# Performance work log

Hardware: AMD Instinct MI355X
Metric: run time of the kernel (lower is better)

## Reference

```python
import jax, jax.numpy as jnp
import numpy as np

B, N, E, H = 32, 256, 768, 12
D = E // H
SCALING = D ** -0.5


def setup_inputs() -> dict:
    key = jax.random.key(0)
    ks = jax.random.split(key, 10)
    inp = {
        "query": jax.random.normal(ks[0], (B, N, E), dtype=jnp.float32),
        "attn_bias": jax.random.normal(ks[1], (B * H, N, N), dtype=jnp.float32),
        "delta_pos": jax.random.normal(ks[2], (B, N, N, 3), dtype=jnp.float32),
        # Linear params stored as (in, out) so y = x @ W + b (equivalent to torch Linear).
        "Wq": jax.random.normal(ks[3], (E, E), dtype=jnp.float32) * 0.02,
        "bq": jnp.zeros((E,), dtype=jnp.float32),
        "Wk": jax.random.normal(ks[4], (E, E), dtype=jnp.float32) * 0.02,
        "bk": jnp.zeros((E,), dtype=jnp.float32),
        "Wv": jax.random.normal(ks[5], (E, E), dtype=jnp.float32) * 0.02,
        "bv": jnp.zeros((E,), dtype=jnp.float32),
        # force_proj: Linear(E, 1, bias=False) -> weight vector (E,)
        "wf": jax.random.normal(ks[6], (E,), dtype=jnp.float32) * 0.02,
    }
    return inp


def reference(query, attn_bias, delta_pos, Wq, bq, Wk, bk, Wv, bv, wf):
    b, n, e = query.shape
    h, d = H, D
    # QKV projections -> (b, n, h, d)
    q = (query @ Wq + bq).reshape(b, n, h, d) * SCALING
    k = (query @ Wk + bk).reshape(b, n, h, d)
    v = (query @ Wv + bv).reshape(b, n, h, d)
    # attention scores (b, h, n, n)
    attn = jnp.einsum("bnhd,bmhd->bhnm", q, k)
    # add bias on flattened (b*h, n, n), softmax over last dim (dropout=0.1 disabled: eval mode)
    probs = jax.nn.softmax(attn.reshape(b * h, n, n) + attn_bias, axis=-1)
    probs = probs.reshape(b, h, n, n)
    # equivariant weighted sum: x[b,n,c,h,d] = sum_m probs[b,h,n,m] * delta_pos[b,n,m,c] * v[b,m,h,d]
    x = jnp.einsum("bhnm,bnmc,bmhd->bnchd", probs, delta_pos, v)
    x = x.reshape(b, n, 3, e)
    # force projection (shared Linear(E,1,bias=False) applied per spatial component)
    force = jnp.einsum("bnce,e->bnc", x, wf).astype(jnp.float32)
    return force
```

## Files before the change

### kernel.cpp

```cpp
#include <hip/hip_runtime.h>
#include <hip/hip_bf16.h>

#define Bc 32
#define Nc 256
#define Ec 768
#define Hc 12
#define Dc 64

typedef __attribute__((ext_vector_type(8))) __bf16 bf16x8;
typedef __attribute__((ext_vector_type(8))) unsigned short u16x8;
typedef __attribute__((ext_vector_type(4))) float f32x4;

__device__ __forceinline__ unsigned short f2bf(float x) {
  union { float f; unsigned u; } v; v.f = x;
  unsigned r = v.u + 0x7fff + ((v.u >> 16) & 1);
  return (unsigned short)(r >> 16);
}

#define GL2LDS(gp, lp) __builtin_amdgcn_global_load_lds( \
    (__attribute__((address_space(1))) void*)(gp),        \
    (__attribute__((address_space(3))) void*)(lp), 16, 0, 0)

__global__ __launch_bounds__(256) void k_trans(const float* __restrict__ Wq,
                                               const float* __restrict__ Wk,
                                               unsigned short* __restrict__ WT) {
  __shared__ float tile[32][33];
  const float* W = blockIdx.z ? Wk : Wq;
  float scale = blockIdx.z ? 1.0f : 0.125f;
  int rowoff = blockIdx.z ? Ec : 0;
  int k0 = blockIdx.x * 32, n0 = blockIdx.y * 32;
  int r = threadIdx.x >> 5, c = threadIdx.x & 31;
  #pragma unroll
  for (int it = 0; it < 4; ++it)
    tile[r + 8 * it][c] = W[(k0 + r + 8 * it) * Ec + n0 + c];
  __syncthreads();
  #pragma unroll
  for (int it = 0; it < 4; ++it)
    WT[(rowoff + n0 + r + 8 * it) * Ec + k0 + c] = f2bf(scale * tile[c][r + 8 * it]);
}

__global__ void k_build_wvf(const float* __restrict__ Wv, const float* __restrict__ bv,
                            const float* __restrict__ wf,
                            const float* __restrict__ bq, const float* __restrict__ bk,
                            float* __restrict__ Wvf, float* __restrict__ bvf,
                            float* __restrict__ bb) {
  int idx = blockIdx.x * 256 + threadIdx.x;
  if (idx < Ec * Hc) {
    int e = idx / Hc, h = idx % Hc;
    float s = 0.f;
    for (int d = 0; d < Dc; ++d) s += Wv[e * Ec + h * Dc + d] * wf[h * Dc + d];
    Wvf[idx] = s;
  }
  if (idx < Hc) {
    float s = 0.f;
    for (int d = 0; d < Dc; ++d) s += bv[idx * Dc + d] * wf[idx * Dc + d];
    bvf[idx] = s;
  }
  if (idx < 2 * Ec)
    bb[idx] = (idx < Ec) ? 0.125f * bq[idx] : bk[idx - Ec];
}

__global__ __launch_bounds__(256) void k_vf(const float* __restrict__ query,
                                            const float* __restrict__ Wvf,
                                            const float* __restrict__ bvf,
                                            float* __restrict__ vfT,
                                            unsigned short* __restrict__ Xb) {
  __shared__ float wl[Ec * 13];
  __shared__ float bl[Hc];
  for (int i = threadIdx.x; i < Ec * Hc; i += 256) {
    int e = i / Hc, h = i % Hc;
    wl[e * 13 + h] = Wvf[i];
  }
  if (threadIdx.x < Hc) bl[threadIdx.x] = bvf[threadIdx.x];
  __syncthreads();
  int warp = threadIdx.x >> 6, lane = threadIdx.x & 63;
  int r = blockIdx.x * 4 + warp;
  float q[12];
  #pragma unroll
  for (int i = 0; i < 12; ++i) q[i] = query[r * Ec + lane + 64 * i];
  #pragma unroll
  for (int i = 0; i < 12; ++i) Xb[r * Ec + lane + 64 * i] = f2bf(q[i]);
  int b = r >> 8, m = r & 255;
  for (int h = 0; h < Hc; ++h) {
    float s = 0.f;
    #pragma unroll
    for (int i = 0; i < 12; ++i) s += q[i] * wl[(lane + 64 * i) * 13 + h];
    #pragma unroll
    for (int off = 32; off; off >>= 1) s += __shfl_xor(s, off);
    if (lane == 0) vfT[(b * Hc + h) * Nc + m] = s + bl[h];
  }
}

__global__ __launch_bounds__(256) void k_gemm_qk(const unsigned short* __restrict__ Xb,
                                                 const unsigned short* __restrict__ WT,
                                                 const float* __restrict__ bb,
                                                 unsigned short* __restrict__ QK) {
  __shared__ unsigned short As[128 * 64];
  __shared__ unsigned short Bs[128 * 64];
  int wgid = (blockIdx.x & 7) * 96 + (blockIdx.x >> 3);
  int bm = wgid & 63, bn = wgid >> 6;
  int t = threadIdx.x;
  int wave = t >> 6, lane = t & 63;
  int wr = wave >> 1, wc = wave & 1;
  int lrow = lane & 15, lq = lane >> 4;
  const int row0 = bm * 128, col0 = bn * 128;

  int srow = wave * 8 + (lane >> 3);
  int soct = (lane & 7);

  f32x4 acc[4][4];
  #pragma unroll
  for (int m = 0; m < 4; ++m)
    #pragma unroll
    for (int n = 0; n < 4; ++n) acc[m][n] = f32x4{0.f, 0.f, 0.f, 0.f};

  for (int ks = 0; ks < Ec; ks += 64) {
    #pragma unroll
    for (int i = 0; i < 4; ++i) {
      int r = i * 32 + srow;
      int go = soct ^ (r & 7);
      GL2LDS(Xb + (row0 + r) * Ec + ks + go * 8, As + i * 2048 + wave * 512);
      GL2LDS(WT + (col0 + r) * Ec + ks + go * 8, Bs + i * 2048 + wave * 512);
    }
    __syncthreads();
    bf16x8 af[4][2], bfg[4][2];
    #pragma unroll
    for (int m = 0; m < 4; ++m) {
      int ra = wr * 64 + m * 16 + lrow;
      #pragma unroll
      for (int kk = 0; kk < 2; ++kk) {
        int o = kk * 4 + lq;
        af[m][kk] = *(const bf16x8*)(As + ra * 64 + ((o ^ (ra & 7)) << 3));
      }
    }
    #pragma unroll
    for (int n = 0; n < 4; ++n) {
      int rb = wc * 64 + n * 16 + lrow;
      #pragma unroll
      for (int kk = 0; kk < 2; ++kk) {
        int o = kk * 4 + lq;
        bfg[n][kk] = *(const bf16x8*)(Bs + rb * 64 + ((o ^ (rb & 7)) << 3));
      }
    }
    #pragma unroll
    for (int kk = 0; kk < 2; ++kk)
      #pragma unroll
      for (int m = 0; m < 4; ++m)
        #pragma unroll
        for (int n = 0; n < 4; ++n)
          acc[m][n] = __builtin_amdgcn_mfma_f32_16x16x32_bf16(af[m][kk], bfg[n][kk], acc[m][n], 0, 0, 0);
    __syncthreads();
  }
  int crow = lq * 4, ccol = lane & 15;
  #pragma unroll
  for (int m = 0; m < 4; ++m)
    #pragma unroll
    for (int n = 0; n < 4; ++n) {
      int col = col0 + wc * 64 + n * 16 + ccol;
      float bias = bb[col];
      #pragma unroll
      for (int j = 0; j < 4; ++j) {
        int row = row0 + wr * 64 + m * 16 + crow + j;
        QK[row * 1536 + col] = f2bf(acc[m][n][j] + bias);
      }
    }
}

__global__ __launch_bounds__(256) void k_attn(const unsigned short* __restrict__ QK,
                                              const float* __restrict__ bias,
                                              const float* __restrict__ vfT,
                                              const float* __restrict__ delta,
                                              float* __restrict__ fpart) {
  __shared__ float S[16 * 256];

  int bi = blockIdx.x;
  int xcd = bi & 7, slot = bi >> 3;
  int b = xcd * 4 + (slot >> 6);
  int rem = slot & 63;
  int nt = rem >> 2, hg = rem & 3;
  int n0 = nt * 16;
  int h0 = hg * 3;

  int t = threadIdx.x, w = t >> 6, l = t & 63;
  int lq = l >> 4, lr = l & 15;

  float w_reg[4][4];
  #pragma unroll
  for (int p = 0; p < 4; ++p)
    #pragma unroll
    for (int i = 0; i < 4; ++i) w_reg[p][i] = 0.f;

  const unsigned short* Qbase = QK + (size_t)b * Nc * 1536;
  const unsigned short* Kbase = Qbase + 768;

  float4 bias4[4], vf4;
  {
    const float* bp = bias + (size_t)(b * Hc + h0) * Nc * Nc;
    #pragma unroll
    for (int p = 0; p < 4; ++p)
      bias4[p] = *(const float4*)(bp + (n0 + w * 4 + p) * Nc + l * 4);
    vf4 = *(const float4*)(vfT + (size_t)(b * Hc + h0) * Nc + l * 4);
  }

  #pragma unroll 1
  for (int hh = 0; hh < 3; ++hh) {
    int h = h0 + hh;
    bf16x8 qf[2];
    #pragma unroll
    for (int kk = 0; kk < 2; ++kk)
      qf[kk] = *(const bf16x8*)(Qbase + (n0 + lr) * 1536 + h * 64 + kk * 32 + lq * 8);
    f32x4 acc[4];
    #pragma unroll
    for (int mf = 0; mf < 4; ++mf) acc[mf] = f32x4{0.f, 0.f, 0.f, 0.f};
    #pragma unroll
    for (int mf = 0; mf < 4; ++mf)
      #pragma unroll
      for (int kk = 0; kk < 2; ++kk) {
        bf16x8 af = *(const bf16x8*)(Kbase + (w * 64 + mf * 16 + lr) * 1536 + h * 64 + kk * 32 + lq * 8);
        acc[mf] = __builtin_amdgcn_mfma_f32_16x16x32_bf16(af, qf[kk], acc[mf], 0, 0, 0);
      }
    float4 bias_nx[4], vf_nx;
    if (hh < 2) {
      const float* bpn = bias + (size_t)(b * Hc + h + 1) * Nc * Nc;
      #pragma unroll
      for (int p = 0; p < 4; ++p)
        bias_nx[p] = *(const float4*)(bpn + (n0 + w * 4 + p) * Nc + l * 4);
      vf_nx = *(const float4*)(vfT + (size_t)(b * Hc + h + 1) * Nc + l * 4);
    }
    #pragma unroll
    for (int mf = 0; mf < 4; ++mf) {
      int m0 = w * 64 + mf * 16 + lq * 4;
      *(f32x4*)&S[lr * 256 + (m0 ^ ((lr & 7) << 2))] = acc[mf];
    }
    __syncthreads();
    #pragma unroll
    for (int p = 0; p < 4; ++p) {
      int r = w * 4 + p;
      float4 sv = *(const float4*)&S[r * 256 + ((l * 4) ^ ((r & 7) << 2))];
      float p0 = __expf(sv.x + bias4[p].x);
      float p1 = __expf(sv.y + bias4[p].y);
      float p2 = __expf(sv.z + bias4[p].z);
      float p3 = __expf(sv.w + bias4[p].w);
      float ssum = (p0 + p1) + (p2 + p3);
      #pragma unroll
      for (int off = 1; off < 64; off <<= 1) ssum += __shfl_xor(ssum, off);
      float inv = 1.f / ssum;
      w_reg[p][0] += p0 * inv * vf4.x;
      w_reg[p][1] += p1 * inv * vf4.y;
      w_reg[p][2] += p2 * inv * vf4.z;
      w_reg[p][3] += p3 * inv * vf4.w;
    }
    __syncthreads();
    if (hh < 2) {
      #pragma unroll
      for (int p = 0; p < 4; ++p) bias4[p] = bias_nx[p];
      vf4 = vf_nx;
    }
  }
  #pragma unroll
  for (int p = 0; p < 4; ++p) {
    int r = w * 4 + p, n = n0 + r;
    const float* dp = delta + ((size_t)(b * Nc + n) * Nc + l * 4) * 3;
    float4 d0 = *(const float4*)(dp);
    float4 d1 = *(const float4*)(dp + 4);
    float4 d2 = *(const float4*)(dp + 8);
    float w0 = w_reg[p][0], w1 = w_reg[p][1], w2 = w_reg[p][2], w3 = w_reg[p][3];
    float f0 = w0 * d0.x + w1 * d0.w + w2 * d1.z + w3 * d2.y;
    float f1 = w0 * d0.y + w1 * d1.x + w2 * d1.w + w3 * d2.z;
    float f2 = w0 * d0.z + w1 * d1.y + w2 * d2.x + w3 * d2.w;
    #pragma unroll
    for (int off = 1; off < 64; off <<= 1) {
      f0 += __shfl_xor(f0, off);
      f1 += __shfl_xor(f1, off);
      f2 += __shfl_xor(f2, off);
    }
    if (l == 0) {
      float4 v; v.x = f0; v.y = f1; v.z = f2; v.w = 0.f;
      *(float4*)(fpart + ((size_t)(hg * Bc + b) * Nc + n) * 4) = v;
    }
  }
}

__global__ __launch_bounds__(256) void k_force(const float* __restrict__ fpart,
                                               float* __restrict__ out) {
  int b = blockIdx.x, n = threadIdx.x;
  float a0 = 0.f, a1 = 0.f, a2 = 0.f;
  #pragma unroll
  for (int g = 0; g < 4; ++g) {
    float4 v = *(const float4*)(fpart + ((size_t)(g * Bc + b) * Nc + n) * 4);
    a0 += v.x; a1 += v.y; a2 += v.z;
  }
  float* o = out + (size_t)(b * Nc + n) * 3;
  o[0] = a0; o[1] = a1; o[2] = a2;
}

extern "C" void kernel_launch(void* const* d_in, const int* in_sizes, int n_in,
                              void* d_out, int out_size, void* d_ws, size_t ws_size,
                              hipStream_t stream) {
  const float* query = (const float*)d_in[0];
  const float* attn_bias = (const float*)d_in[1];
  const float* delta_pos = (const float*)d_in[2];
  const float* Wq = (const float*)d_in[3];
  const float* bq = (const float*)d_in[4];
  const float* Wk = (const float*)d_in[5];
  const float* bk = (const float*)d_in[6];
  const float* Wv = (const float*)d_in[7];
  const float* bv = (const float*)d_in[8];
  const float* wf = (const float*)d_in[9];
  float* out = (float*)d_out;

  char* ws = (char*)d_ws;
  unsigned short* WT  = (unsigned short*)(ws);
  unsigned short* QKb = (unsigned short*)(ws + 2359296);
  unsigned short* Xb  = (unsigned short*)(ws + 27525120);
  float* fpart = (float*)(ws + 27525120);
  float* vfT = (float*)(ws + 40108032);
  float* Wvf = (float*)(ws + 40501248);
  float* bvf = (float*)(ws + 40538112);
  float* bb  = (float*)(ws + 40538160);

  k_trans<<<dim3(24, 24, 2), 256, 0, stream>>>(Wq, Wk, WT);
  k_build_wvf<<<36, 256, 0, stream>>>(Wv, bv, wf, bq, bk, Wvf, bvf, bb);
  k_vf<<<2048, 256, 0, stream>>>(query, Wvf, bvf, vfT, Xb);
  k_gemm_qk<<<768, 256, 0, stream>>>(Xb, WT, bb, QKb);
  k_attn<<<2048, 256, 0, stream>>>(QKb, attn_bias, vfT, delta_pos, fpart);
  k_force<<<Bc, 256, 0, stream>>>(fpart, out);
}
```

Measured before the change: 127.5 us.

## Process four heads per attention block and stage bias into LDS asynchronously

Each attention block now covers four heads instead of three, so the grid shrinks to 1536 blocks and the force kernel sums three head-group partials instead of four. This cuts how often delta_pos is re-read and lowers the number of partial outputs. The per-head attention bias is prefetched straight into a double-buffered LDS tile with global_load_lds, replacing the register prefetch. The synchronisation is hand-rolled with raw barriers and lgkmcnt waits, and LDS use grows to about 48KB per block, which may reduce occupancy.

```diff
diff --git a/kernel.cpp b/kernel.cpp
--- a/kernel.cpp
+++ b/kernel.cpp
@@ -172,14 +172,15 @@
                                               const float* __restrict__ delta,
                                               float* __restrict__ fpart) {
   __shared__ float S[16 * 256];
+  __shared__ float Bb[2][16 * 256];
 
   int bi = blockIdx.x;
   int xcd = bi & 7, slot = bi >> 3;
-  int b = xcd * 4 + (slot >> 6);
-  int rem = slot & 63;
-  int nt = rem >> 2, hg = rem & 3;
+  int b = xcd * 4 + slot / 48;
+  int rem = slot % 48;
+  int nt = rem / 3, hg = rem % 3;
   int n0 = nt * 16;
-  int h0 = hg * 3;
+  int h0 = hg * 4;
 
   int t = threadIdx.x, w = t >> 6, l = t & 63;
   int lq = l >> 4, lr = l & 15;
@@ -193,17 +194,16 @@
   const unsigned short* Qbase = QK + (size_t)b * Nc * 1536;
   const unsigned short* Kbase = Qbase + 768;
 
-  float4 bias4[4], vf4;
   {
-    const float* bp = bias + (size_t)(b * Hc + h0) * Nc * Nc;
-    #pragma unroll
-    for (int p = 0; p < 4; ++p)
-      bias4[p] = *(const float4*)(bp + (n0 + w * 4 + p) * Nc + l * 4);
-    vf4 = *(const float4*)(vfT + (size_t)(b * Hc + h0) * Nc + l * 4);
-  }
+    const float* g = bias + ((size_t)(b * Hc + h0) * Nc + n0) * Nc;
+    #pragma unroll
+    for (int i = 0; i < 4; ++i)
+      GL2LDS(g + (w * 4 + i) * 256 + l * 4, &Bb[0][(w * 4 + i) * 256]);
+  }
+  float4 vf4 = *(const float4*)(vfT + (size_t)(b * Hc + h0) * Nc + l * 4);
 
   #pragma unroll 1
-  for (int hh = 0; hh < 3; ++hh) {
+  for (int hh = 0; hh < 4; ++hh) {
     int h = h0 + hh;
     bf16x8 qf[2];
     #pragma unroll
@@ -219,28 +219,32 @@
         bf16x8 af = *(const bf16x8*)(Kbase + (w * 64 + mf * 16 + lr) * 1536 + h * 64 + kk * 32 + lq * 8);
         acc[mf] = __builtin_amdgcn_mfma_f32_16x16x32_bf16(af, qf[kk], acc[mf], 0, 0, 0);
       }
-    float4 bias_nx[4], vf_nx;
-    if (hh < 2) {
-      const float* bpn = bias + (size_t)(b * Hc + h + 1) * Nc * Nc;
-      #pragma unroll
-      for (int p = 0; p < 4; ++p)
-        bias_nx[p] = *(const float4*)(bpn + (n0 + w * 4 + p) * Nc + l * 4);
-      vf_nx = *(const float4*)(vfT + (size_t)(b * Hc + h + 1) * Nc + l * 4);
-    }
     #pragma unroll
     for (int mf = 0; mf < 4; ++mf) {
       int m0 = w * 64 + mf * 16 + lq * 4;
       *(f32x4*)&S[lr * 256 + (m0 ^ ((lr & 7) << 2))] = acc[mf];
     }
-    __syncthreads();
+    asm volatile("s_waitcnt lgkmcnt(0)" ::: "memory");
+    __builtin_amdgcn_sched_barrier(0);
+    __builtin_amdgcn_s_barrier();
+    float4 vf_nx;
+    if (hh < 3) {
+      const float* g = bias + ((size_t)(b * Hc + h + 1) * Nc + n0) * Nc;
+      #pragma unroll
+      for (int i = 0; i < 4; ++i)
+        GL2LDS(g + (w * 4 + i) * 256 + l * 4, &Bb[(hh + 1) & 1][(w * 4 + i) * 256]);
+      vf_nx = *(const float4*)(vfT + (size_t)(b * Hc + h + 1) * Nc + l * 4);
+    }
+    const float* Bcur = &Bb[hh & 1][0];
     #pragma unroll
     for (int p = 0; p < 4; ++p) {
       int r = w * 4 + p;
       float4 sv = *(const float4*)&S[r * 256 + ((l * 4) ^ ((r & 7) << 2))];
-      float p0 = __expf(sv.x + bias4[p].x);
-      float p1 = __expf(sv.y + bias4[p].y);
-      float p2 = __expf(sv.z + bias4[p].z);
-      float p3 = __expf(sv.w + bias4[p].w);
+      float4 bv = *(const float4*)&Bcur[r * 256 + l * 4];
+      float p0 = __expf(sv.x + bv.x);
+      float p1 = __expf(sv.y + bv.y);
+      float p2 = __expf(sv.z + bv.z);
+      float p3 = __expf(sv.w + bv.w);
       float ssum = (p0 + p1) + (p2 + p3);
       #pragma unroll
       for (int off = 1; off < 64; off <<= 1) ssum += __shfl_xor(ssum, off);
@@ -250,12 +254,8 @@
       w_reg[p][2] += p2 * inv * vf4.z;
       w_reg[p][3] += p3 * inv * vf4.w;
     }
-    __syncthreads();
-    if (hh < 2) {
-      #pragma unroll
-      for (int p = 0; p < 4; ++p) bias4[p] = bias_nx[p];
-      vf4 = vf_nx;
-    }
+    __builtin_amdgcn_s_barrier();
+    if (hh < 3) vf4 = vf_nx;
   }
   #pragma unroll
   for (int p = 0; p < 4; ++p) {
@@ -286,7 +286,7 @@
   int b = blockIdx.x, n = threadIdx.x;
   float a0 = 0.f, a1 = 0.f, a2 = 0.f;
   #pragma unroll
-  for (int g = 0; g < 4; ++g) {
+  for (int g = 0; g < 3; ++g) {
     float4 v = *(const float4*)(fpart + ((size_t)(g * Bc + b) * Nc + n) * 4);
     a0 += v.x; a1 += v.y; a2 += v.z;
   }
@@ -323,6 +323,6 @@
   k_build_wvf<<<36, 256, 0, stream>>>(Wv, bv, wf, bq, bk, Wvf, bvf, bb);
   k_vf<<<2048, 256, 0, stream>>>(query, Wvf, bvf, vfT, Xb);
   k_gemm_qk<<<768, 256, 0, stream>>>(Xb, WT, bb, QKb);
-  k_attn<<<2048, 256, 0, stream>>>(QKb, attn_bias, vfT, delta_pos, fpart);
+  k_attn<<<1536, 256, 0, stream>>>(QKb, attn_bias, vfT, delta_pos, fpart);
   k_force<<<Bc, 256, 0, stream>>>(fpart, out);
 }
```

Result: faster. 122.1 us (-4.2%).
